# Kernel tuning notes

Measured on AMD Instinct MI355X. Metric: run time of the kernel, lower is better.

The kernel has to match this reference:

```python
import jax, jax.numpy as jnp
import numpy as np

VOCAB = 500000
EMBED = 64
RANK = 8
# tensor_shape computed by _calculate_tensor_shape(500000, 64): factors of 32e6 -> (2, 4, 4000000)
D0, D1, D2 = 2, 4, 4000000


def setup_inputs() -> dict:
    key = jax.random.key(0)
    k0, k1, k2, k3 = jax.random.split(key, 4)
    core0 = jax.random.normal(k0, (1, D0, RANK), dtype=jnp.float32)
    core1 = jax.random.normal(k1, (RANK, D1, RANK), dtype=jnp.float32)
    core2 = jax.random.normal(k2, (RANK, D2, 1), dtype=jnp.float32)
    input_ids = jax.random.randint(k3, (16, 512), 0, VOCAB, dtype=jnp.int64)
    return {"input_ids": input_ids, "core0": core0, "core1": core1, "core2": core2}


def reference(input_ids, core0, core1, core2):
    # TT-core chain contraction into the full dense table (as the torch module
    # does every forward), then a standard embedding gather.
    # core0: (1, D0, R), core1: (R, D1, R) -> (1, D0, D1, R) -> (D0*D1, R)
    left = jnp.einsum('aib,bjc->aijc', core0, core1).reshape(D0 * D1, RANK)
    # (D0*D1, R) @ (R, D2) -> full tensor (D0*D1, D2) == (VOCAB*EMBED) elems
    table = (left @ core2.reshape(RANK, D2)).reshape(VOCAB, EMBED)
    return table[input_ids]  # [batch, seq_len, embed_dim]
```

## Files before the change

### kernel.cpp

```cpp
#include <hip/hip_runtime.h>


#define TT_D0   2
#define TT_D1   4
#define TT_D2   4000000
#define TT_RANK 8
#define TT_NTOK (16 * 512)
#define TT_EMB  64
#define TT_VDIV 62500

__global__ __launch_bounds__(256) void TTEmbeddingLayer_84713934946739_kernel(
    const int*   __restrict__ ids,
    const float* __restrict__ core0,
    const float* __restrict__ core1,
    const float* __restrict__ core2,
    float*       __restrict__ out)
{
    __shared__ float left[TT_D0 * TT_D1][TT_RANK];

    const int tid = threadIdx.x;

    if (tid < TT_D0 * TT_D1 * TT_RANK) {
        const int c  = tid & (TT_RANK - 1);
        const int ij = tid >> 3;
        const int i0 = ij / TT_D1;
        const int i1 = ij - i0 * TT_D1;
        float s = 0.f;
#pragma unroll
        for (int b = 0; b < TT_RANK; ++b)
            s += core0[i0 * TT_RANK + b] * core1[(b * TT_D1 + i1) * TT_RANK + c];
        left[ij][c] = s;
    }
    __syncthreads();

    const int wave = tid >> 6;
    const int lane = tid & 63;
    const int tok  = blockIdx.x * 4 + wave;
    if (tok >= TT_NTOK) return;

    const int v    = ids[tok];
    const int i    = v / TT_VDIV;
    const int base = (v - i * TT_VDIV) * TT_EMB + lane;

    float acc = 0.f;
#pragma unroll
    for (int r = 0; r < TT_RANK; ++r)
        acc += left[i][r] * core2[r * TT_D2 + base];

    out[tok * TT_EMB + lane] = acc;
}

extern "C" void kernel_launch(void* const* d_in, const int* in_sizes, int n_in,
                              void* d_out, int out_size, void* d_ws, size_t ws_size,
                              hipStream_t stream) {
    const int*   ids   = (const int*)  d_in[0];
    const float* core0 = (const float*)d_in[1];
    const float* core1 = (const float*)d_in[2];
    const float* core2 = (const float*)d_in[3];
    float*       out   = (float*)      d_out;

    const int blocks = TT_NTOK / 4;
    TTEmbeddingLayer_84713934946739_kernel<<<blocks, 256, 0, stream>>>(
        ids, core0, core1, core2, out);
}
```

Baseline: 9.518 us.

## Process four tokens per wave and issue core2 gathers before the left-matrix barrier

Each wave now handles four tokens instead of one, and the launch uses a quarter as many blocks. All 32 core2 loads per lane are issued before the shared-memory core0×core1 contraction and its barrier, so their latency overlaps that setup. Token ids are made wave-uniform with readfirstlane, and the per-block left-matrix recomputation is amortized over more tokens. The cost is higher register use and fewer blocks to spread across CUs. The bounds check on the token index is dropped and the left array is resized to 8x8.

```diff
diff --git a/kernel.cpp b/kernel.cpp
--- a/kernel.cpp
+++ b/kernel.cpp
@@ -1,13 +1,14 @@
 #include <hip/hip_runtime.h>
 
 
-#define TT_D0   2
 #define TT_D1   4
 #define TT_D2   4000000
 #define TT_RANK 8
 #define TT_NTOK (16 * 512)
 #define TT_EMB  64
 #define TT_VDIV 62500
+#define T_PW    4
+#define WPB     4
 
 __global__ __launch_bounds__(256) void TTEmbeddingLayer_84713934946739_kernel(
     const int*   __restrict__ ids,
@@ -16,15 +17,36 @@
     const float* __restrict__ core2,
     float*       __restrict__ out)
 {
-    __shared__ float left[TT_D0 * TT_D1][TT_RANK];
+    __shared__ float left[TT_RANK][TT_RANK];
 
-    const int tid = threadIdx.x;
+    const int tid  = threadIdx.x;
+    const int lane = tid & 63;
+    const int wave = tid >> 6;
+    const int tokbase = (blockIdx.x * WPB + wave) * T_PW;
 
-    if (tid < TT_D0 * TT_D1 * TT_RANK) {
+    int v[T_PW];
+#pragma unroll
+    for (int t = 0; t < T_PW; ++t)
+        v[t] = ids[tokbase + t];
+
+    int   li[T_PW];
+    float x[T_PW][TT_RANK];
+#pragma unroll
+    for (int t = 0; t < T_PW; ++t) {
+        const int vv = __builtin_amdgcn_readfirstlane(v[t]);
+        const int i  = vv / TT_VDIV;
+        li[t] = i;
+        const int base = (vv - i * TT_VDIV) * TT_EMB + lane;
+#pragma unroll
+        for (int r = 0; r < TT_RANK; ++r)
+            x[t][r] = core2[r * TT_D2 + base];
+    }
+
+    if (tid < TT_RANK * TT_RANK) {
         const int c  = tid & (TT_RANK - 1);
         const int ij = tid >> 3;
-        const int i0 = ij / TT_D1;
-        const int i1 = ij - i0 * TT_D1;
+        const int i0 = ij >> 2;
+        const int i1 = ij & 3;
         float s = 0.f;
 #pragma unroll
         for (int b = 0; b < TT_RANK; ++b)
@@ -33,21 +55,14 @@
     }
     __syncthreads();
 
-    const int wave = tid >> 6;
-    const int lane = tid & 63;
-    const int tok  = blockIdx.x * 4 + wave;
-    if (tok >= TT_NTOK) return;
-
-    const int v    = ids[tok];
-    const int i    = v / TT_VDIV;
-    const int base = (v - i * TT_VDIV) * TT_EMB + lane;
-
-    float acc = 0.f;
 #pragma unroll
-    for (int r = 0; r < TT_RANK; ++r)
-        acc += left[i][r] * core2[r * TT_D2 + base];
-
-    out[tok * TT_EMB + lane] = acc;
+    for (int t = 0; t < T_PW; ++t) {
+        float acc = 0.f;
+#pragma unroll
+        for (int r = 0; r < TT_RANK; ++r)
+            acc += left[li[t]][r] * x[t][r];
+        out[(tokbase + t) * TT_EMB + lane] = acc;
+    }
 }
 
 extern "C" void kernel_launch(void* const* d_in, const int* in_sizes, int n_in,
@@ -59,7 +74,7 @@
     const float* core2 = (const float*)d_in[3];
     float*       out   = (float*)      d_out;
 
-    const int blocks = TT_NTOK / 4;
+    const int blocks = TT_NTOK / (T_PW * WPB);
     TTEmbeddingLayer_84713934946739_kernel<<<blocks, 256, 0, stream>>>(
         ids, core0, core1, core2, out);
 }
```

Measured after the change: 9.586 us. No clear change (+0.7%).
